# Optimization experiments

Measured on AMD Instinct MI355X. Metric: run time of the kernel, lower is better.

## Reference

```python
import jax, jax.numpy as jnp
import numpy as np

# Matches neurite/SynthSeg Resize layer: output coord i maps to input coord i/zoom,
# multilinear interpolation with edge clipping (neurite interpn 'linear').
# Multilinear interp is separable, so we apply exact 1-D linear interpolation per axis.
ZOOM = (1.5, 1.5, 1.5)


def _interp_linear_axis(vol, zoom, axis):
    d = vol.shape[axis]
    size_out = int(d * zoom)
    # sample locations in input space: loc = i / zoom  (neurite: grid + (grid/zoom - grid))
    loc = jnp.arange(size_out, dtype=jnp.float32) / jnp.float32(zoom)
    maxd = jnp.float32(d - 1)
    cloc = jnp.clip(loc, 0.0, maxd)                     # clipped continuous location
    i0 = jnp.clip(jnp.floor(loc), 0.0, maxd).astype(jnp.int32)
    i1 = jnp.clip(i0 + 1, 0, d - 1)
    # neurite convention: weight of lower corner = loc1 - clipped_loc
    w0 = i1.astype(jnp.float32) - cloc
    w1 = 1.0 - w0
    bshape = [1] * vol.ndim
    bshape[axis] = size_out
    w0 = w0.reshape(bshape)
    w1 = w1.reshape(bshape)
    return jnp.take(vol, i0, axis=axis) * w0 + jnp.take(vol, i1, axis=axis) * w1


def reference(vol):
    # vol: [B, D, H, W, C] -> [B, D*1.5, H*1.5, W*1.5, C]
    out = vol
    for dim, z in enumerate(ZOOM):
        out = _interp_linear_axis(out, z, axis=dim + 1)  # skip batch axis
    return out


def setup_inputs() -> dict:
    key = jax.random.key(0)
    vol = jax.random.normal(key, (2, 128, 128, 128, 2), dtype=jnp.float32)
    return {"vol": vol}
```

## Files before the change

kernel.cpp:

```cpp
#include <hip/hip_runtime.h>

constexpr int B = 2, D = 128, H = 128, W = 128;
constexpr int OD = 192, OH = 192, OW = 192;

__device__ __forceinline__ void axis_interp(int i, int d, int& i0, int& i1, float& w0) {
    float loc  = (float)i * (1.0f / 1.5f);
    float maxd = (float)(d - 1);
    float cloc = fminf(loc, maxd);
    float f    = fminf(floorf(loc), maxd);
    i0 = (int)f;
    i1 = (i0 + 1 < d) ? (i0 + 1) : (d - 1);
    w0 = (float)i1 - cloc;
}

__global__ __launch_bounds__(256)
void resize_trilinear3(const float2* __restrict__ in, float2* __restrict__ out) {
    const int t = threadIdx.x;
    const int y = blockIdx.x * 4 + threadIdx.y;
    const int z = blockIdx.y;
    const int b = blockIdx.z;

    int z0, z1, y0, y1;
    float wz0, wy0;
    axis_interp(z, D, z0, z1, wz0);
    axis_interp(y, H, y0, y1, wy0);
    const float wz1 = 1.f - wz0, wy1 = 1.f - wy0;

    const float2* base = in + (size_t)b * (D * H * W);
    const float2* r00 = base + (z0 * H + y0) * W + 2 * t;
    const float2* r01 = base + (z0 * H + y1) * W + 2 * t;
    const float2* r10 = base + (z1 * H + y0) * W + 2 * t;
    const float2* r11 = base + (z1 * H + y1) * W + 2 * t;
    const int e2 = (t < 63) ? 2 : 1;

    float2 v00a = r00[0], v00b = r00[1], v00c = r00[e2];
    float2 v01a = r01[0], v01b = r01[1], v01c = r01[e2];
    float2 v10a = r10[0], v10b = r10[1], v10c = r10[e2];
    float2 v11a = r11[0], v11b = r11[1], v11c = r11[e2];

    float c0x = wz0 * (wy0 * v00a.x + wy1 * v01a.x) + wz1 * (wy0 * v10a.x + wy1 * v11a.x);
    float c0y = wz0 * (wy0 * v00a.y + wy1 * v01a.y) + wz1 * (wy0 * v10a.y + wy1 * v11a.y);
    float c1x = wz0 * (wy0 * v00b.x + wy1 * v01b.x) + wz1 * (wy0 * v10b.x + wy1 * v11b.x);
    float c1y = wz0 * (wy0 * v00b.y + wy1 * v01b.y) + wz1 * (wy0 * v10b.y + wy1 * v11b.y);
    float c2x = wz0 * (wy0 * v00c.x + wy1 * v01c.x) + wz1 * (wy0 * v10c.x + wy1 * v11c.x);
    float c2y = wz0 * (wy0 * v00c.y + wy1 * v01c.y) + wz1 * (wy0 * v10c.y + wy1 * v11c.y);

    constexpr float W13 = 1.0f / 3.0f, W23 = 2.0f / 3.0f;
    float2 o0, o1, o2;
    o0.x = c0x;
    o0.y = c0y;
    o1.x = W13 * c0x + W23 * c1x;
    o1.y = W13 * c0y + W23 * c1y;
    o2.x = W23 * c1x + W13 * c2x;
    o2.y = W23 * c1y + W13 * c2y;

    float2* orow = out + (((size_t)b * OD + z) * OH + y) * OW + 3 * t;
    orow[0] = o0;
    orow[1] = o1;
    orow[2] = o2;
}

extern "C" void kernel_launch(void* const* d_in, const int* in_sizes, int n_in,
                              void* d_out, int out_size, void* d_ws, size_t ws_size,
                              hipStream_t stream) {
    const float2* in = (const float2*)d_in[0];
    float2* out = (float2*)d_out;
    dim3 block(64, 4, 1);
    dim3 grid(OH / 4, OD, B);
    resize_trilinear3<<<grid, block, 0, stream>>>(in, out);
}
```

Baseline: 32.46 us.

## Compute a full 3x3x3 output block per thread from a 3x3x3 input patch

Each thread now loads a 3x3x3 input neighbourhood and writes 27 output voxels, using the fact that zoom 1.5 maps every two input voxels to three outputs with fixed 1/3 and 2/3 weights. This cuts redundant input reads across output rows and planes, and removes the per-output index and weight computation. The grid shrinks by nine times, so there is less parallelism and more registers per thread, and each thread's stores are strided across three rows and three planes.

```diff
diff --git a/kernel.cpp b/kernel.cpp
--- a/kernel.cpp
+++ b/kernel.cpp
@@ -3,61 +3,77 @@
 constexpr int B = 2, D = 128, H = 128, W = 128;
 constexpr int OD = 192, OH = 192, OW = 192;
 
-__device__ __forceinline__ void axis_interp(int i, int d, int& i0, int& i1, float& w0) {
-    float loc  = (float)i * (1.0f / 1.5f);
-    float maxd = (float)(d - 1);
-    float cloc = fminf(loc, maxd);
-    float f    = fminf(floorf(loc), maxd);
-    i0 = (int)f;
-    i1 = (i0 + 1 < d) ? (i0 + 1) : (d - 1);
-    w0 = (float)i1 - cloc;
+__device__ __forceinline__ float2 lerp13(float2 u, float2 v) {
+    constexpr float A = 1.0f / 3.0f, Bc = 2.0f / 3.0f;
+    return float2{A * u.x + Bc * v.x, A * u.y + Bc * v.y};
+}
+__device__ __forceinline__ float2 lerp23(float2 u, float2 v) {
+    constexpr float A = 1.0f / 3.0f, Bc = 2.0f / 3.0f;
+    return float2{Bc * u.x + A * v.x, Bc * u.y + A * v.y};
+}
+
+__device__ __forceinline__ void load_patch(const float2* __restrict__ plane,
+                                           int iy, int yc, int ix, int xc,
+                                           float2 m[3][3]) {
+    const float2* r0 = plane + (size_t)iy * W;
+    const float2* r1 = r0 + W;
+    const float2* r2 = plane + (size_t)yc * W;
+    m[0][0] = r0[ix]; m[0][1] = r0[ix + 1]; m[0][2] = r0[xc];
+    m[1][0] = r1[ix]; m[1][1] = r1[ix + 1]; m[1][2] = r1[xc];
+    m[2][0] = r2[ix]; m[2][1] = r2[ix + 1]; m[2][2] = r2[xc];
+}
+
+__device__ __forceinline__ void xy_store(const float2 m[3][3], float2* __restrict__ o) {
+    float2 t0[3], t1[3], t2[3];
+    t0[0] = m[0][0]; t0[1] = lerp13(m[0][0], m[0][1]); t0[2] = lerp23(m[0][1], m[0][2]);
+    t1[0] = m[1][0]; t1[1] = lerp13(m[1][0], m[1][1]); t1[2] = lerp23(m[1][1], m[1][2]);
+    t2[0] = m[2][0]; t2[1] = lerp13(m[2][0], m[2][1]); t2[2] = lerp23(m[2][1], m[2][2]);
+    o[0] = t0[0]; o[1] = t0[1]; o[2] = t0[2];
+    float2* o1 = o + OW;
+    o1[0] = lerp13(t0[0], t1[0]); o1[1] = lerp13(t0[1], t1[1]); o1[2] = lerp13(t0[2], t1[2]);
+    float2* o2 = o + 2 * OW;
+    o2[0] = lerp23(t1[0], t2[0]); o2[1] = lerp23(t1[1], t2[1]); o2[2] = lerp23(t1[2], t2[2]);
 }
 
 __global__ __launch_bounds__(256)
-void resize_trilinear3(const float2* __restrict__ in, float2* __restrict__ out) {
-    const int t = threadIdx.x;
-    const int y = blockIdx.x * 4 + threadIdx.y;
-    const int z = blockIdx.y;
+void resize27(const float2* __restrict__ in, float2* __restrict__ out) {
+    const int X = threadIdx.x;
+    const int Y = blockIdx.x * 4 + threadIdx.y;
+    const int Z = blockIdx.y;
     const int b = blockIdx.z;
 
-    int z0, z1, y0, y1;
-    float wz0, wy0;
-    axis_interp(z, D, z0, z1, wz0);
-    axis_interp(y, H, y0, y1, wy0);
-    const float wz1 = 1.f - wz0, wy1 = 1.f - wy0;
+    const int ix = 2 * X, iy = 2 * Y, iz = 2 * Z;
+    const int xc = (ix + 2 < W) ? ix + 2 : W - 1;
+    const int yc = (iy + 2 < H) ? iy + 2 : H - 1;
+    const int zc = (iz + 2 < D) ? iz + 2 : D - 1;
 
     const float2* base = in + (size_t)b * (D * H * W);
-    const float2* r00 = base + (z0 * H + y0) * W + 2 * t;
-    const float2* r01 = base + (z0 * H + y1) * W + 2 * t;
-    const float2* r10 = base + (z1 * H + y0) * W + 2 * t;
-    const float2* r11 = base + (z1 * H + y1) * W + 2 * t;
-    const int e2 = (t < 63) ? 2 : 1;
+    const float2* p0 = base + (size_t)iz * (H * W);
+    const float2* p1 = base + (size_t)(iz + 1) * (H * W);
+    const float2* p2 = base + (size_t)zc * (H * W);
 
-    float2 v00a = r00[0], v00b = r00[1], v00c = r00[e2];
-    float2 v01a = r01[0], v01b = r01[1], v01c = r01[e2];
-    float2 v10a = r10[0], v10b = r10[1], v10c = r10[e2];
-    float2 v11a = r11[0], v11b = r11[1], v11c = r11[e2];
+    float2 m0[3][3], m1[3][3], m2[3][3];
+    load_patch(p0, iy, yc, ix, xc, m0);
+    load_patch(p1, iy, yc, ix, xc, m1);
+    load_patch(p2, iy, yc, ix, xc, m2);
 
-    float c0x = wz0 * (wy0 * v00a.x + wy1 * v01a.x) + wz1 * (wy0 * v10a.x + wy1 * v11a.x);
-    float c0y = wz0 * (wy0 * v00a.y + wy1 * v01a.y) + wz1 * (wy0 * v10a.y + wy1 * v11a.y);
-    float c1x = wz0 * (wy0 * v00b.x + wy1 * v01b.x) + wz1 * (wy0 * v10b.x + wy1 * v11b.x);
-    float c1y = wz0 * (wy0 * v00b.y + wy1 * v01b.y) + wz1 * (wy0 * v10b.y + wy1 * v11b.y);
-    float c2x = wz0 * (wy0 * v00c.x + wy1 * v01c.x) + wz1 * (wy0 * v10c.x + wy1 * v11c.x);
-    float c2y = wz0 * (wy0 * v00c.y + wy1 * v01c.y) + wz1 * (wy0 * v10c.y + wy1 * v11c.y);
+    float2* ob = out + (((size_t)b * OD + 3 * Z) * OH + 3 * Y) * OW + 3 * X;
+    constexpr size_t ZS = (size_t)OH * OW;
 
-    constexpr float W13 = 1.0f / 3.0f, W23 = 2.0f / 3.0f;
-    float2 o0, o1, o2;
-    o0.x = c0x;
-    o0.y = c0y;
-    o1.x = W13 * c0x + W23 * c1x;
-    o1.y = W13 * c0y + W23 * c1y;
-    o2.x = W23 * c1x + W13 * c2x;
-    o2.y = W23 * c1y + W13 * c2y;
+    xy_store(m0, ob);
 
-    float2* orow = out + (((size_t)b * OD + z) * OH + y) * OW + 3 * t;
-    orow[0] = o0;
-    orow[1] = o1;
-    orow[2] = o2;
+    float2 q[3][3];
+#pragma unroll
+    for (int i = 0; i < 3; ++i)
+#pragma unroll
+        for (int j = 0; j < 3; ++j) q[i][j] = lerp13(m0[i][j], m1[i][j]);
+    xy_store(q, ob + ZS);
+
+#pragma unroll
+    for (int i = 0; i < 3; ++i)
+#pragma unroll
+        for (int j = 0; j < 3; ++j) q[i][j] = lerp23(m1[i][j], m2[i][j]);
+    xy_store(q, ob + 2 * ZS);
 }
 
 extern "C" void kernel_launch(void* const* d_in, const int* in_sizes, int n_in,
@@ -66,6 +82,6 @@
     const float2* in = (const float2*)d_in[0];
     float2* out = (float2*)d_out;
     dim3 block(64, 4, 1);
-    dim3 grid(OH / 4, OD, B);
-    resize_trilinear3<<<grid, block, 0, stream>>>(in, out);
+    dim3 grid(16, 64, B);
+    resize27<<<grid, block, 0, stream>>>(in, out);
 }
```

Measured after the change: 38.69 us. 19.2% more time.
